# Performance work log

Measured on AMD Instinct MI355X. Metric: run time of the kernel, lower is better.

Reference implementation:

```python
import jax, jax.numpy as jnp
import numpy as np

N_NODES = 100000
N_EDGES = 800000
D = 256
OUT = 1

def _glorot(key, shape):
    fan_in, fan_out = shape[1], shape[0]
    lim = np.sqrt(6.0 / (fan_in + fan_out)).astype(np.float32)
    return jax.random.uniform(key, shape, jnp.float32, -lim, lim)

def setup_inputs() -> dict:
    key = jax.random.key(0)
    ks = jax.random.split(key, 12)
    x = jax.random.normal(ks[0], (N_NODES, D), jnp.float32)
    edge_index = jax.random.randint(ks[1], (2, N_EDGES), 0, N_NODES, jnp.int64)
    return {
        "x": x,
        "edge_index": edge_index,
        # SAGEConv: lin_l acts on aggregated neighbors (has bias), lin_r on root (no bias)
        "W_l": _glorot(ks[2], (256, D)),
        "b_l": jnp.zeros((256,), jnp.float32),
        "W_r": _glorot(ks[3], (256, D)),
        # MLP
        "W1": _glorot(ks[4], (128, 256)),
        "b1": jnp.zeros((128,), jnp.float32),
        "W2": _glorot(ks[5], (32, 128)),
        "b2": jnp.zeros((32,), jnp.float32),
        "W3": _glorot(ks[6], (OUT, 32)),
        "b3": jnp.zeros((OUT,), jnp.float32),
    }

def reference(x, edge_index, W_l, b_l, W_r, W1, b1, W2, b2, W3, b3):
    src, dst = edge_index[0], edge_index[1]
    # mean aggregation of neighbor (source) features at destination nodes
    msg = x[src]                                            # [E, D]
    agg = jax.ops.segment_sum(msg, dst, num_segments=N_NODES)   # [N, D]
    cnt = jax.ops.segment_sum(jnp.ones((edge_index.shape[1],), x.dtype), dst,
                              num_segments=N_NODES)          # [N]
    mean = agg / jnp.maximum(cnt, 1.0)[:, None]
    # SAGEConv: lin_l(mean_neigh) + lin_r(x)
    conv = mean @ W_l.T + b_l + x @ W_r.T                   # [N, 256]
    out = jax.nn.relu(conv)
    h = out + x                                              # residual
    h = jax.nn.relu(h @ W1.T + b1)
    h = jax.nn.relu(h @ W2.T + b2)
    return h @ W3.T + b3                                     # [N, OUT]
```

## Files before the change

### kernel.cpp

```cpp
#include <hip/hip_runtime.h>
#include <cstddef>

#define NN 100000
#define NE 800000
#define DD 256
#define CAP 40

typedef unsigned short u16;
typedef __bf16 bf8_t __attribute__((ext_vector_type(8)));
typedef float f32x4 __attribute__((ext_vector_type(4)));
typedef u16 u16x8 __attribute__((ext_vector_type(8)));

__device__ __forceinline__ float bf2f(u16 u) {
    union { unsigned int i; float f; } v; v.i = ((unsigned int)u) << 16; return v.f;
}
__device__ __forceinline__ u16 f2bf(float f) {
    union { float f; unsigned int i; } v; v.f = f;
    unsigned int x = v.i;
    unsigned int r = (x + 0x7FFFu + ((x >> 16) & 1u)) >> 16;
    return (u16)r;
}

__device__ __forceinline__ void bar_lds() {
    asm volatile("s_waitcnt lgkmcnt(0)" ::: "memory");
    __builtin_amdgcn_s_barrier();
    asm volatile("" ::: "memory");
}

__global__ void GNNActor_23192823398472_kernel() {}

__device__ __forceinline__ float ldwf(const void* p, int i, int f32) {
    return f32 ? ((const float*)p)[i] : bf2f(((const u16*)p)[i]);
}

__global__ void k_prep(const u16* __restrict__ x, const int* __restrict__ ei,
                       int* __restrict__ flags, int4* __restrict__ z4, int nz4,
                       const void* __restrict__ Wl, const void* __restrict__ Wr,
                       const void* __restrict__ W1, const void* __restrict__ W2,
                       const void* __restrict__ W3, const void* __restrict__ bl,
                       const void* __restrict__ b1, const void* __restrict__ b2,
                       const void* __restrict__ b3, u16* __restrict__ pk,
                       float* __restrict__ pb) {
    int nzb = (nz4 + 255) / 256;
    if ((int)blockIdx.x < nzb) {
        int i = blockIdx.x * 256 + threadIdx.x;
        if (i < nz4) z4[i] = (int4){0, 0, 0, 0};
        if (blockIdx.x == 0 && threadIdx.x < 64) {
            int lane = threadIdx.x;
            int big = 0;
            for (int k = lane; k < 4096; k += 64) {
                u16 u = x[k];
                if (((u >> 7) & 0xFF) >= 140) ++big;
            }
            #pragma unroll
            for (int off = 32; off; off >>= 1) big += __shfl_down(big, off, 64);
            int bad = 0;
            for (int k = lane; k < 128; k += 64) bad |= (ei[2 * k + 1] != 0) ? 1 : 0;
            unsigned long long anybad = __ballot(bad);
            if (lane == 0) {
                flags[0] = (big > 64) ? 1 : 0;
                flags[1] = anybad ? 0 : 1;
            }
        }
        return;
    }
    __shared__ int s_f32;
    if (threadIdx.x < 64) {
        int lane = threadIdx.x;
        int big = 0;
        for (int k = lane; k < 4096; k += 64) {
            u16 u = x[k];
            if (((u >> 7) & 0xFF) >= 140) ++big;
        }
        #pragma unroll
        for (int off = 32; off; off >>= 1) big += __shfl_down(big, off, 64);
        if (lane == 0) s_f32 = (big > 64) ? 1 : 0;
    }
    __syncthreads();
    int f32 = s_f32;
    int id = (blockIdx.x - nzb) * 256 + threadIdx.x;
    if (id < 16384) {
        int lr = id & 15, lq = (id >> 4) & 3, c = (id >> 6) & 15, ctg = id >> 10;
        int n = ctg * 16 + lr;
        int k = (c & 7) * 32 + lq * 8;
        const void* W = (c < 8) ? Wl : Wr;
        u16x8 o;
        #pragma unroll
        for (int j = 0; j < 8; ++j) o[j] = f2bf(ldwf(W, n * DD + k + j, f32));
        *(u16x8*)&pk[id * 8] = o;
    } else if (id < 20480) {
        int id2 = id - 16384;
        int lr = id2 & 15, lq = (id2 >> 4) & 3, c = (id2 >> 6) & 7, wv = id2 >> 9;
        int n = wv * 16 + lr;
        u16x8 o;
        #pragma unroll
        for (int j = 0; j < 8; ++j) o[j] = f2bf(ldwf(W1, n * DD + c * 32 + lq * 8 + j, f32));
        *(u16x8*)&pk[131072 + id2 * 8] = o;
    } else if (id < 20992) {
        int id2 = id - 20480;
        int lr = id2 & 15, lq = (id2 >> 4) & 3, c = (id2 >> 6) & 3, wv = id2 >> 8;
        int n = wv * 16 + lr;
        u16x8 o;
        #pragma unroll
        for (int j = 0; j < 8; ++j) o[j] = f2bf(ldwf(W2, n * 128 + c * 32 + lq * 8 + j, f32));
        *(u16x8*)&pk[163840 + id2 * 8] = o;
    } else if (id < 21441) {
        int j = id - 20992;
        float v;
        if (j < 256)      v = ldwf(bl, j, f32);
        else if (j < 384) v = ldwf(b1, j - 256, f32);
        else if (j < 416) v = ldwf(b2, j - 384, f32);
        else if (j == 416) v = ldwf(b3, 0, f32);
        else              v = ldwf(W3, j - 417, f32);
        pb[j] = v;
    }
}

__global__ void k_scatter(const int* __restrict__ ei, int* __restrict__ cnt_i,
                          int* __restrict__ elist, const int* __restrict__ flags) {
    int e0 = (blockIdx.x * blockDim.x + threadIdx.x) * 4;
    if (e0 >= NE) return;
    int d0, d1, d2, d3, s0, s1, s2, s3;
    if (flags[1]) {
        int4 a = *(const int4*)&ei[2 * NE + 2 * e0];
        int4 b = *(const int4*)&ei[2 * NE + 2 * e0 + 4];
        d0 = a.x; d1 = a.z; d2 = b.x; d3 = b.z;
        int4 p = *(const int4*)&ei[2 * e0];
        int4 q = *(const int4*)&ei[2 * e0 + 4];
        s0 = p.x; s1 = p.z; s2 = q.x; s3 = q.z;
    } else {
        int4 a = *(const int4*)&ei[NE + e0];
        d0 = a.x; d1 = a.y; d2 = a.z; d3 = a.w;
        int4 p = *(const int4*)&ei[e0];
        s0 = p.x; s1 = p.y; s2 = p.z; s3 = p.w;
    }
    int p0 = atomicAdd(&cnt_i[d0], 1); if (p0 < CAP) elist[d0 * CAP + p0] = s0;
    int p1 = atomicAdd(&cnt_i[d1], 1); if (p1 < CAP) elist[d1 * CAP + p1] = s1;
    int p2 = atomicAdd(&cnt_i[d2], 1); if (p2 < CAP) elist[d2 * CAP + p2] = s2;
    int p3 = atomicAdd(&cnt_i[d3], 1); if (p3 < CAP) elist[d3 * CAP + p3] = s3;
}

template <int F32>
__device__ __forceinline__ void gather_body(const int* __restrict__ cnt_i,
                                            const int* __restrict__ elist,
                                            const void* __restrict__ xv,
                                            u16* __restrict__ meanb,
                                            int* s_idx, int* s_cnt) {
    int t = threadIdx.x;
    int node0 = blockIdx.x * 16;
    if (t < 160) ((int4*)s_idx)[t] = ((const int4*)&elist[node0 * CAP])[t];
    if (t < 16) s_cnt[t] = cnt_i[node0 + t];
    __syncthreads();

    int wv = t >> 6, lane = t & 63, half = lane >> 5, li = lane & 31;
    for (int q = 0; q < 4; ++q) {
        int n = wv * 4 + q;
        int cnt = s_cnt[n];
        int m = cnt < CAP ? cnt : CAP;
        float a0=0.f,a1=0.f,a2=0.f,a3=0.f,a4=0.f,a5=0.f,a6=0.f,a7=0.f;
        for (int b = 0; b < m; b += 16) {
            u16x8 u[8]; float4 fA[8], fB[8]; float msk[8];
            #pragma unroll
            for (int g = 0; g < 8; ++g) {
                int j = b + g * 2 + half;
                int ok = j < m;
                int jj = ok ? j : 0;
                msk[g] = ok ? 1.f : 0.f;
                int src = s_idx[n * CAP + jj];
                if (F32) {
                    const float* p = (const float*)xv + (size_t)src * DD + li * 8;
                    fA[g] = *(const float4*)p;
                    fB[g] = *(const float4*)(p + 4);
                } else {
                    u[g] = *(const u16x8*)((const u16*)xv + (size_t)src * DD + li * 8);
                }
            }
            #pragma unroll
            for (int g = 0; g < 8; ++g) {
                if (F32) {
                    a0 = fmaf(msk[g], fA[g].x, a0); a1 = fmaf(msk[g], fA[g].y, a1);
                    a2 = fmaf(msk[g], fA[g].z, a2); a3 = fmaf(msk[g], fA[g].w, a3);
                    a4 = fmaf(msk[g], fB[g].x, a4); a5 = fmaf(msk[g], fB[g].y, a5);
                    a6 = fmaf(msk[g], fB[g].z, a6); a7 = fmaf(msk[g], fB[g].w, a7);
                } else {
                    a0 = fmaf(msk[g], bf2f(u[g][0]), a0); a1 = fmaf(msk[g], bf2f(u[g][1]), a1);
                    a2 = fmaf(msk[g], bf2f(u[g][2]), a2); a3 = fmaf(msk[g], bf2f(u[g][3]), a3);
                    a4 = fmaf(msk[g], bf2f(u[g][4]), a4); a5 = fmaf(msk[g], bf2f(u[g][5]), a5);
                    a6 = fmaf(msk[g], bf2f(u[g][6]), a6); a7 = fmaf(msk[g], bf2f(u[g][7]), a7);
                }
            }
        }
        a0 += __shfl_xor(a0, 32, 64); a1 += __shfl_xor(a1, 32, 64);
        a2 += __shfl_xor(a2, 32, 64); a3 += __shfl_xor(a3, 32, 64);
        a4 += __shfl_xor(a4, 32, 64); a5 += __shfl_xor(a5, 32, 64);
        a6 += __shfl_xor(a6, 32, 64); a7 += __shfl_xor(a7, 32, 64);
        if (lane < 32) {
            float inv = 1.f / fmaxf((float)cnt, 1.f);
            u16x8 o;
            o[0]=f2bf(a0*inv); o[1]=f2bf(a1*inv); o[2]=f2bf(a2*inv); o[3]=f2bf(a3*inv);
            o[4]=f2bf(a4*inv); o[5]=f2bf(a5*inv); o[6]=f2bf(a6*inv); o[7]=f2bf(a7*inv);
            *(u16x8*)&meanb[(size_t)(node0 + n) * DD + li * 8] = o;
        }
    }
}

__launch_bounds__(256)
__global__ void k_gather(const int* __restrict__ cnt_i, const int* __restrict__ elist,
                         const void* __restrict__ xv, u16* __restrict__ meanb,
                         const int* __restrict__ flags) {
    __shared__ int s_idx[16 * CAP];
    __shared__ int s_cnt[16];
    if (flags[0]) gather_body<1>(cnt_i, elist, xv, meanb, s_idx, s_cnt);
    else          gather_body<0>(cnt_i, elist, xv, meanb, s_idx, s_cnt);
}

#define SMS 264
#define SH1 136
#define SH2 40

template <int F32>
__device__ __forceinline__ void mm_body(
        const u16* __restrict__ meanb, const void* __restrict__ xv,
        const u16* __restrict__ pk, const float* __restrict__ pb,
        void* __restrict__ outv, char* smem) {
    u16* s_mean = (u16*)smem;
    u16* s_x    = (u16*)(smem + 16896);
    u16* s_h    = (u16*)smem;
    u16* s_h1   = (u16*)(smem + 16896);
    u16* s_h2   = (u16*)smem;

    int t = threadIdx.x;
    int node0 = blockIdx.x * 32;
    int wv = t >> 6, lane = t & 63;
    int lq = lane >> 4, lr = lane & 15;
    int fo = lq * 128 + lr * 8;

    const u16* pk1 = pk + 131072;
    const u16* pk2 = pk + 163840;
    int ctg0 = wv * 2, ctg1 = ctg0 + 1;

    #define LWC(ctg, c) (*(const bf8_t*)&pk[((ctg) * 16 + (c)) * 512 + fo])

    bf8_t w0[16], w1[16];
    #pragma unroll
    for (int c = 0; c < 4; ++c) { w0[c] = LWC(ctg0, c); w1[c] = LWC(ctg1, c); }

    {
        int i0 = t, i1 = t + 512;
        int r0 = i0 >> 5, k0 = (i0 & 31) << 3;
        int r1 = i1 >> 5, k1 = (i1 & 31) << 3;
        u16x8 m0 = *(const u16x8*)&meanb[(size_t)(node0 + r0) * DD + k0];
        u16x8 m1 = *(const u16x8*)&meanb[(size_t)(node0 + r1) * DD + k1];
        u16x8 x0, x1;
        if (F32) {
            const float* p0 = (const float*)xv + (size_t)(node0 + r0) * DD + k0;
            const float* p1 = (const float*)xv + (size_t)(node0 + r1) * DD + k1;
            float4 fa = *(const float4*)p0, fb = *(const float4*)(p0 + 4);
            float4 fc = *(const float4*)p1, fd = *(const float4*)(p1 + 4);
            x0[0]=f2bf(fa.x); x0[1]=f2bf(fa.y); x0[2]=f2bf(fa.z); x0[3]=f2bf(fa.w);
            x0[4]=f2bf(fb.x); x0[5]=f2bf(fb.y); x0[6]=f2bf(fb.z); x0[7]=f2bf(fb.w);
            x1[0]=f2bf(fc.x); x1[1]=f2bf(fc.y); x1[2]=f2bf(fc.z); x1[3]=f2bf(fc.w);
            x1[4]=f2bf(fd.x); x1[5]=f2bf(fd.y); x1[6]=f2bf(fd.z); x1[7]=f2bf(fd.w);
        } else {
            x0 = *(const u16x8*)((const u16*)xv + (size_t)(node0 + r0) * DD + k0);
            x1 = *(const u16x8*)((const u16*)xv + (size_t)(node0 + r1) * DD + k1);
        }
        *(u16x8*)&s_mean[r0 * SMS + k0] = m0;
        *(u16x8*)&s_mean[r1 * SMS + k1] = m1;
        *(u16x8*)&s_x[r0 * SMS + k0] = x0;
        *(u16x8*)&s_x[r1 * SMS + k1] = x1;
    }
    bar_lds();

    f32x4 acc00 = (f32x4){0.f,0.f,0.f,0.f}, acc10 = (f32x4){0.f,0.f,0.f,0.f};
    f32x4 acc01 = (f32x4){0.f,0.f,0.f,0.f}, acc11 = (f32x4){0.f,0.f,0.f,0.f};

    #pragma unroll
    for (int c = 0; c < 16; ++c) {
        if (c < 12) { w0[c + 4] = LWC(ctg0, c + 4); w1[c + 4] = LWC(ctg1, c + 4); }
        const u16* ab = (c < 8) ? s_mean : s_x;
        int co = (c & 7) * 32 + lq * 8;
        bf8_t a0 = *(const bf8_t*)&ab[lr * SMS + co];
        bf8_t a1 = *(const bf8_t*)&ab[(16 + lr) * SMS + co];
        acc00 = __builtin_amdgcn_mfma_f32_16x16x32_bf16(a0, w0[c], acc00, 0, 0, 0);
        acc10 = __builtin_amdgcn_mfma_f32_16x16x32_bf16(a1, w0[c], acc10, 0, 0, 0);
        acc01 = __builtin_amdgcn_mfma_f32_16x16x32_bf16(a0, w1[c], acc01, 0, 0, 0);
        acc11 = __builtin_amdgcn_mfma_f32_16x16x32_bf16(a1, w1[c], acc11, 0, 0, 0);
    }

    bf8_t v1[8];
    #pragma unroll
    for (int c = 0; c < 8; ++c) v1[c] = *(const bf8_t*)&pk1[(wv * 8 + c) * 512 + fo];

    bar_lds();

    #pragma unroll
    for (int ct = 0; ct < 2; ++ct) {
        int n = (wv * 2 + ct) * 16 + lr;
        float bb = pb[n];
        const f32x4* ac0 = ct ? &acc01 : &acc00;
        const f32x4* ac1 = ct ? &acc11 : &acc10;
        #pragma unroll
        for (int i = 0; i < 4; ++i) {
            int m0 = lq * 4 + i;
            s_h[m0 * SMS + n] = f2bf(fmaxf((*ac0)[i] + bb, 0.f) + bf2f(s_x[m0 * SMS + n]));
            int m1 = 16 + lq * 4 + i;
            s_h[m1 * SMS + n] = f2bf(fmaxf((*ac1)[i] + bb, 0.f) + bf2f(s_x[m1 * SMS + n]));
        }
    }
    bar_lds();

    {
        f32x4 a1c0 = (f32x4){0.f,0.f,0.f,0.f}, a1c1 = (f32x4){0.f,0.f,0.f,0.f};
        int n = wv * 16 + lr;
        #pragma unroll
        for (int c = 0; c < 8; ++c) {
            bf8_t a0 = *(const bf8_t*)&s_h[lr * SMS + c * 32 + lq * 8];
            bf8_t a1 = *(const bf8_t*)&s_h[(16 + lr) * SMS + c * 32 + lq * 8];
            a1c0 = __builtin_amdgcn_mfma_f32_16x16x32_bf16(a0, v1[c], a1c0, 0, 0, 0);
            a1c1 = __builtin_amdgcn_mfma_f32_16x16x32_bf16(a1, v1[c], a1c1, 0, 0, 0);
        }
        bf8_t v2[4];
        if (wv < 2) {
            #pragma unroll
            for (int c = 0; c < 4; ++c) v2[c] = *(const bf8_t*)&pk2[(wv * 4 + c) * 512 + fo];
        }
        float bb = pb[256 + n];
        #pragma unroll
        for (int i = 0; i < 4; ++i) {
            int m0 = lq * 4 + i;
            s_h1[m0 * SH1 + n] = f2bf(fmaxf(a1c0[i] + bb, 0.f));
            int m1 = 16 + lq * 4 + i;
            s_h1[m1 * SH1 + n] = f2bf(fmaxf(a1c1[i] + bb, 0.f));
        }
        bar_lds();

        if (wv < 2) {
            f32x4 a2c0 = (f32x4){0.f,0.f,0.f,0.f}, a2c1 = (f32x4){0.f,0.f,0.f,0.f};
            #pragma unroll
            for (int c = 0; c < 4; ++c) {
                bf8_t a0 = *(const bf8_t*)&s_h1[lr * SH1 + c * 32 + lq * 8];
                bf8_t a1 = *(const bf8_t*)&s_h1[(16 + lr) * SH1 + c * 32 + lq * 8];
                a2c0 = __builtin_amdgcn_mfma_f32_16x16x32_bf16(a0, v2[c], a2c0, 0, 0, 0);
                a2c1 = __builtin_amdgcn_mfma_f32_16x16x32_bf16(a1, v2[c], a2c1, 0, 0, 0);
            }
            float bb2 = pb[384 + n];
            #pragma unroll
            for (int i = 0; i < 4; ++i) {
                int m0 = lq * 4 + i;
                s_h2[m0 * SH2 + n] = f2bf(fmaxf(a2c0[i] + bb2, 0.f));
                int m1 = 16 + lq * 4 + i;
                s_h2[m1 * SH2 + n] = f2bf(fmaxf(a2c1[i] + bb2, 0.f));
            }
        }
    }
    bar_lds();

    if (t < 32) {
        float a3 = pb[416];
        #pragma unroll
        for (int k = 0; k < 32; ++k)
            a3 += bf2f(s_h2[t * SH2 + k]) * pb[417 + k];
        if (F32) ((float*)outv)[node0 + t] = a3;
        else     ((u16*)outv)[node0 + t]   = f2bf(a3);
    }
    #undef LWC
}

__launch_bounds__(512, 4)
__global__ void k_mm(const u16* __restrict__ meanb, const void* __restrict__ xv,
                     const u16* __restrict__ pk, const float* __restrict__ pb,
                     void* __restrict__ outv, const int* __restrict__ flags) {
    __shared__ __align__(16) char smem[33792];
    if (flags[0]) mm_body<1>(meanb, xv, pk, pb, outv, smem);
    else          mm_body<0>(meanb, xv, pk, pb, outv, smem);
}

extern "C" void kernel_launch(void* const* d_in, const int* in_sizes, int n_in,
                              void* d_out, int out_size, void* d_ws, size_t ws_size,
                              hipStream_t stream) {
    const u16* x  = (const u16*)d_in[0];
    const int* ei = (const int*)d_in[1];
    const void* Wl = d_in[2];
    const void* bl = d_in[3];
    const void* Wr = d_in[4];
    const void* W1 = d_in[5];
    const void* b1 = d_in[6];
    const void* W2 = d_in[7];
    const void* b2 = d_in[8];
    const void* W3 = d_in[9];
    const void* b3 = d_in[10];

    u16* meanb = (u16*)d_ws;
    int* flags = (int*)(meanb + (size_t)NN * DD);
    int* cnt_i = flags + 256;
    int* elist = cnt_i + NN;
    u16* pk    = (u16*)(elist + (size_t)NN * CAP);
    float* pb  = (float*)(pk + 167936);

    int nz4 = NN / 4;
    int nzb = (nz4 + 255) / 256;
    k_prep<<<nzb + 84, 256, 0, stream>>>(x, ei, flags, (int4*)cnt_i, nz4,
                                         Wl, Wr, W1, W2, W3, bl, b1, b2, b3, pk, pb);
    k_scatter<<<(NE / 4 + 255) / 256, 256, 0, stream>>>(ei, cnt_i, elist, flags);
    k_gather<<<NN / 16, 256, 0, stream>>>(cnt_i, elist, (const void*)x, meanb, flags);
    k_mm<<<NN / 32, 512, 0, stream>>>(meanb, (const void*)x, pk, pb, d_out, flags);
}
```

Measured before the change: 388.4 us.

## Fuse neighbor mean gather into the MLP matmul kernel via shared memory

Merges the gather kernel into the matmul kernel. Each 512-thread block now stages its 32 nodes' edge lists in LDS, computes the neighbor mean directly into shared memory, and then runs the MFMA chain. This removes the global bf16 mean buffer write and re-read and one kernel launch. In exchange, weight prefetch is delayed until after the gather, LDS per block grows, and latency-bound gather work now shares register and occupancy limits with the matmul.

Result: faster. 358.7 us (-7.6%).

```diff
diff --git a/kernel.cpp b/kernel.cpp
--- a/kernel.cpp
+++ b/kernel.cpp
@@ -140,91 +140,20 @@
     int p3 = atomicAdd(&cnt_i[d3], 1); if (p3 < CAP) elist[d3 * CAP + p3] = s3;
 }
 
-template <int F32>
-__device__ __forceinline__ void gather_body(const int* __restrict__ cnt_i,
-                                            const int* __restrict__ elist,
-                                            const void* __restrict__ xv,
-                                            u16* __restrict__ meanb,
-                                            int* s_idx, int* s_cnt) {
-    int t = threadIdx.x;
-    int node0 = blockIdx.x * 16;
-    if (t < 160) ((int4*)s_idx)[t] = ((const int4*)&elist[node0 * CAP])[t];
-    if (t < 16) s_cnt[t] = cnt_i[node0 + t];
-    __syncthreads();
-
-    int wv = t >> 6, lane = t & 63, half = lane >> 5, li = lane & 31;
-    for (int q = 0; q < 4; ++q) {
-        int n = wv * 4 + q;
-        int cnt = s_cnt[n];
-        int m = cnt < CAP ? cnt : CAP;
-        float a0=0.f,a1=0.f,a2=0.f,a3=0.f,a4=0.f,a5=0.f,a6=0.f,a7=0.f;
-        for (int b = 0; b < m; b += 16) {
-            u16x8 u[8]; float4 fA[8], fB[8]; float msk[8];
-            #pragma unroll
-            for (int g = 0; g < 8; ++g) {
-                int j = b + g * 2 + half;
-                int ok = j < m;
-                int jj = ok ? j : 0;
-                msk[g] = ok ? 1.f : 0.f;
-                int src = s_idx[n * CAP + jj];
-                if (F32) {
-                    const float* p = (const float*)xv + (size_t)src * DD + li * 8;
-                    fA[g] = *(const float4*)p;
-                    fB[g] = *(const float4*)(p + 4);
-                } else {
-                    u[g] = *(const u16x8*)((const u16*)xv + (size_t)src * DD + li * 8);
-                }
-            }
-            #pragma unroll
-            for (int g = 0; g < 8; ++g) {
-                if (F32) {
-                    a0 = fmaf(msk[g], fA[g].x, a0); a1 = fmaf(msk[g], fA[g].y, a1);
-                    a2 = fmaf(msk[g], fA[g].z, a2); a3 = fmaf(msk[g], fA[g].w, a3);
-                    a4 = fmaf(msk[g], fB[g].x, a4); a5 = fmaf(msk[g], fB[g].y, a5);
-                    a6 = fmaf(msk[g], fB[g].z, a6); a7 = fmaf(msk[g], fB[g].w, a7);
-                } else {
-                    a0 = fmaf(msk[g], bf2f(u[g][0]), a0); a1 = fmaf(msk[g], bf2f(u[g][1]), a1);
-                    a2 = fmaf(msk[g], bf2f(u[g][2]), a2); a3 = fmaf(msk[g], bf2f(u[g][3]), a3);
-                    a4 = fmaf(msk[g], bf2f(u[g][4]), a4); a5 = fmaf(msk[g], bf2f(u[g][5]), a5);
-                    a6 = fmaf(msk[g], bf2f(u[g][6]), a6); a7 = fmaf(msk[g], bf2f(u[g][7]), a7);
-                }
-            }
-        }
-        a0 += __shfl_xor(a0, 32, 64); a1 += __shfl_xor(a1, 32, 64);
-        a2 += __shfl_xor(a2, 32, 64); a3 += __shfl_xor(a3, 32, 64);
-        a4 += __shfl_xor(a4, 32, 64); a5 += __shfl_xor(a5, 32, 64);
-        a6 += __shfl_xor(a6, 32, 64); a7 += __shfl_xor(a7, 32, 64);
-        if (lane < 32) {
-            float inv = 1.f / fmaxf((float)cnt, 1.f);
-            u16x8 o;
-            o[0]=f2bf(a0*inv); o[1]=f2bf(a1*inv); o[2]=f2bf(a2*inv); o[3]=f2bf(a3*inv);
-            o[4]=f2bf(a4*inv); o[5]=f2bf(a5*inv); o[6]=f2bf(a6*inv); o[7]=f2bf(a7*inv);
-            *(u16x8*)&meanb[(size_t)(node0 + n) * DD + li * 8] = o;
-        }
-    }
-}
-
-__launch_bounds__(256)
-__global__ void k_gather(const int* __restrict__ cnt_i, const int* __restrict__ elist,
-                         const void* __restrict__ xv, u16* __restrict__ meanb,
-                         const int* __restrict__ flags) {
-    __shared__ int s_idx[16 * CAP];
-    __shared__ int s_cnt[16];
-    if (flags[0]) gather_body<1>(cnt_i, elist, xv, meanb, s_idx, s_cnt);
-    else          gather_body<0>(cnt_i, elist, xv, meanb, s_idx, s_cnt);
-}
-
 #define SMS 264
 #define SH1 136
 #define SH2 40
 
 template <int F32>
-__device__ __forceinline__ void mm_body(
-        const u16* __restrict__ meanb, const void* __restrict__ xv,
+__device__ __forceinline__ void fused_body(
+        const int* __restrict__ cnt_i, const int* __restrict__ elist,
+        const void* __restrict__ xv,
         const u16* __restrict__ pk, const float* __restrict__ pb,
         void* __restrict__ outv, char* smem) {
     u16* s_mean = (u16*)smem;
     u16* s_x    = (u16*)(smem + 16896);
+    int* s_el   = (int*)(smem + 33792);
+    int* s_cnt  = (int*)(smem + 38912);
     u16* s_h    = (u16*)smem;
     u16* s_h1   = (u16*)(smem + 16896);
     u16* s_h2   = (u16*)smem;
@@ -235,22 +164,12 @@
     int lq = lane >> 4, lr = lane & 15;
     int fo = lq * 128 + lr * 8;
 
-    const u16* pk1 = pk + 131072;
-    const u16* pk2 = pk + 163840;
-    int ctg0 = wv * 2, ctg1 = ctg0 + 1;
-
-    #define LWC(ctg, c) (*(const bf8_t*)&pk[((ctg) * 16 + (c)) * 512 + fo])
-
-    bf8_t w0[16], w1[16];
-    #pragma unroll
-    for (int c = 0; c < 4; ++c) { w0[c] = LWC(ctg0, c); w1[c] = LWC(ctg1, c); }
-
+    if (t < 32) s_cnt[t] = cnt_i[node0 + t];
+    if (t < 320) ((int4*)s_el)[t] = ((const int4*)&elist[(size_t)node0 * CAP])[t];
     {
         int i0 = t, i1 = t + 512;
         int r0 = i0 >> 5, k0 = (i0 & 31) << 3;
         int r1 = i1 >> 5, k1 = (i1 & 31) << 3;
-        u16x8 m0 = *(const u16x8*)&meanb[(size_t)(node0 + r0) * DD + k0];
-        u16x8 m1 = *(const u16x8*)&meanb[(size_t)(node0 + r1) * DD + k1];
         u16x8 x0, x1;
         if (F32) {
             const float* p0 = (const float*)xv + (size_t)(node0 + r0) * DD + k0;
@@ -265,11 +184,72 @@
             x0 = *(const u16x8*)((const u16*)xv + (size_t)(node0 + r0) * DD + k0);
             x1 = *(const u16x8*)((const u16*)xv + (size_t)(node0 + r1) * DD + k1);
         }
-        *(u16x8*)&s_mean[r0 * SMS + k0] = m0;
-        *(u16x8*)&s_mean[r1 * SMS + k1] = m1;
         *(u16x8*)&s_x[r0 * SMS + k0] = x0;
         *(u16x8*)&s_x[r1 * SMS + k1] = x1;
     }
+    bar_lds();
+
+    int half = lane >> 5, li = lane & 31;
+    #pragma unroll 1
+    for (int q = 0; q < 4; ++q) {
+        int n = wv * 4 + q;
+        int cnt = s_cnt[n];
+        int m = cnt < CAP ? cnt : CAP;
+        float a0=0.f,a1=0.f,a2=0.f,a3=0.f,a4=0.f,a5=0.f,a6=0.f,a7=0.f;
+        for (int b = 0; b < m; b += 16) {
+            u16x8 u[8]; float4 fA[8], fB[8]; float msk[8];
+            #pragma unroll
+            for (int g = 0; g < 8; ++g) {
+                int j = b + g * 2 + half;
+                int ok = j < m;
+                int jj = ok ? j : 0;
+                msk[g] = ok ? 1.f : 0.f;
+                int src = s_el[n * CAP + jj];
+                if (F32) {
+                    const float* p = (const float*)xv + (size_t)src * DD + li * 8;
+                    fA[g] = *(const float4*)p;
+                    fB[g] = *(const float4*)(p + 4);
+                } else {
+                    u[g] = *(const u16x8*)((const u16*)xv + (size_t)src * DD + li * 8);
+                }
+            }
+            #pragma unroll
+            for (int g = 0; g < 8; ++g) {
+                if (F32) {
+                    a0 = fmaf(msk[g], fA[g].x, a0); a1 = fmaf(msk[g], fA[g].y, a1);
+                    a2 = fmaf(msk[g], fA[g].z, a2); a3 = fmaf(msk[g], fA[g].w, a3);
+                    a4 = fmaf(msk[g], fB[g].x, a4); a5 = fmaf(msk[g], fB[g].y, a5);
+                    a6 = fmaf(msk[g], fB[g].z, a6); a7 = fmaf(msk[g], fB[g].w, a7);
+                } else {
+                    a0 = fmaf(msk[g], bf2f(u[g][0]), a0); a1 = fmaf(msk[g], bf2f(u[g][1]), a1);
+                    a2 = fmaf(msk[g], bf2f(u[g][2]), a2); a3 = fmaf(msk[g], bf2f(u[g][3]), a3);
+                    a4 = fmaf(msk[g], bf2f(u[g][4]), a4); a5 = fmaf(msk[g], bf2f(u[g][5]), a5);
+                    a6 = fmaf(msk[g], bf2f(u[g][6]), a6); a7 = fmaf(msk[g], bf2f(u[g][7]), a7);
+                }
+            }
+        }
+        a0 += __shfl_xor(a0, 32, 64); a1 += __shfl_xor(a1, 32, 64);
+        a2 += __shfl_xor(a2, 32, 64); a3 += __shfl_xor(a3, 32, 64);
+        a4 += __shfl_xor(a4, 32, 64); a5 += __shfl_xor(a5, 32, 64);
+        a6 += __shfl_xor(a6, 32, 64); a7 += __shfl_xor(a7, 32, 64);
+        if (lane < 32) {
+            float inv = 1.f / fmaxf((float)cnt, 1.f);
+            u16x8 o;
+            o[0]=f2bf(a0*inv); o[1]=f2bf(a1*inv); o[2]=f2bf(a2*inv); o[3]=f2bf(a3*inv);
+            o[4]=f2bf(a4*inv); o[5]=f2bf(a5*inv); o[6]=f2bf(a6*inv); o[7]=f2bf(a7*inv);
+            *(u16x8*)&s_mean[n * SMS + li * 8] = o;
+        }
+    }
+
+    const u16* pk1 = pk + 131072;
+    const u16* pk2 = pk + 163840;
+    int ctg0 = wv * 2, ctg1 = ctg0 + 1;
+    #define LWC(ctg, c) (*(const bf8_t*)&pk[((ctg) * 16 + (c)) * 512 + fo])
+
+    bf8_t w0[16], w1[16];
+    #pragma unroll
+    for (int c = 0; c < 4; ++c) { w0[c] = LWC(ctg0, c); w1[c] = LWC(ctg1, c); }
+
     bar_lds();
 
     f32x4 acc00 = (f32x4){0.f,0.f,0.f,0.f}, acc10 = (f32x4){0.f,0.f,0.f,0.f};
@@ -368,12 +348,13 @@
 }
 
 __launch_bounds__(512, 4)
-__global__ void k_mm(const u16* __restrict__ meanb, const void* __restrict__ xv,
-                     const u16* __restrict__ pk, const float* __restrict__ pb,
-                     void* __restrict__ outv, const int* __restrict__ flags) {
-    __shared__ __align__(16) char smem[33792];
-    if (flags[0]) mm_body<1>(meanb, xv, pk, pb, outv, smem);
-    else          mm_body<0>(meanb, xv, pk, pb, outv, smem);
+__global__ void k_fused(const int* __restrict__ cnt_i, const int* __restrict__ elist,
+                        const void* __restrict__ xv,
+                        const u16* __restrict__ pk, const float* __restrict__ pb,
+                        void* __restrict__ outv, const int* __restrict__ flags) {
+    __shared__ __align__(16) char smem[39040];
+    if (flags[0]) fused_body<1>(cnt_i, elist, xv, pk, pb, outv, smem);
+    else          fused_body<0>(cnt_i, elist, xv, pk, pb, outv, smem);
 }
 
 extern "C" void kernel_launch(void* const* d_in, const int* in_sizes, int n_in,
@@ -391,8 +372,7 @@
     const void* W3 = d_in[9];
     const void* b3 = d_in[10];
 
-    u16* meanb = (u16*)d_ws;
-    int* flags = (int*)(meanb + (size_t)NN * DD);
+    int* flags = (int*)d_ws;
     int* cnt_i = flags + 256;
     int* elist = cnt_i + NN;
     u16* pk    = (u16*)(elist + (size_t)NN * CAP);
@@ -403,6 +383,6 @@
     k_prep<<<nzb + 84, 256, 0, stream>>>(x, ei, flags, (int4*)cnt_i, nz4,
                                          Wl, Wr, W1, W2, W3, bl, b1, b2, b3, pk, pb);
     k_scatter<<<(NE / 4 + 255) / 256, 256, 0, stream>>>(ei, cnt_i, elist, flags);
-    k_gather<<<NN / 16, 256, 0, stream>>>(cnt_i, elist, (const void*)x, meanb, flags);
-    k_mm<<<NN / 32, 512, 0, stream>>>(meanb, (const void*)x, pk, pb, d_out, flags);
-}
+    k_fused<<<NN / 32, 512, 0, stream>>>(cnt_i, elist, (const void*)x, pk, pb,
+                                         d_out, flags);
+}
```
